# Optimization experiments

Hardware: AMD Instinct MI355X
Metric: run time of the kernel (lower is better)

## Reference

```python
import jax, jax.numpy as jnp
import numpy as np

B, NUM_OBJ, R, D, C = 1024, 128, 32, 512, 7  # scans, obj slots, rel samples, feat dim, rel classes
N = NUM_OBJ + R  # 160 graph nodes per scan


def setup_inputs() -> dict:
    key = jax.random.key(0)
    ks = jax.random.split(key, 8)
    obj_feats = jax.random.normal(ks[0], (B, NUM_OBJ, D), jnp.float32)
    pairs = jax.random.randint(ks[1], (B, R, 2), 0, NUM_OBJ, dtype=jnp.int32)
    init = lambda k, shape, fan_in: jax.random.normal(k, shape, jnp.float32) / np.float32(np.sqrt(fan_in))
    return {
        "obj_feats": obj_feats,
        "pairs": pairs,
        "fuse_w": init(ks[2], (2 * D, D), 2 * D), "fuse_b": jnp.zeros((D,), jnp.float32),
        "gcn_w": init(ks[3], (D, D), D), "gcn_b": jnp.zeros((D,), jnp.float32),
        "fc1_w": init(ks[4], (D, 256), D), "fc1_b": jnp.zeros((256,), jnp.float32),
        "fc2_w": init(ks[5], (256, 128), 256), "fc2_b": jnp.zeros((128,), jnp.float32),
        "fc3_w": init(ks[6], (128, C), 128), "fc3_b": jnp.zeros((C,), jnp.float32),
    }


def reference(obj_feats, pairs, fuse_w, fuse_b, gcn_w, gcn_b,
              fc1_w, fc1_b, fc2_w, fc2_b, fc3_w, fc3_b):
    # --- init_rel_node (pos_fuse=False): fuse sub/obj features per sampled pair ---
    sub = jnp.take_along_axis(obj_feats, pairs[:, :, 0:1], axis=1)  # [B,R,D]
    obj = jnp.take_along_axis(obj_feats, pairs[:, :, 1:2], axis=1)  # [B,R,D]
    init_rel = jnp.concatenate([sub, obj], axis=-1) @ fuse_w + fuse_b  # [B,R,D]

    # --- X: object node feats in rows [0,NUM_OBJ), rel node feats in rows [NUM_OBJ,N) ---
    X = jnp.concatenate([obj_feats, init_rel], axis=1)  # [B,N,D]

    # --- A: get_graph_gcn_with_rel -- scatter 4 directed edges per pair ---
    b_idx = jnp.arange(B)[:, None]                      # [B,1]
    ridx = NUM_OBJ + jnp.arange(R)[None, :]             # [1,R] rel node index j+num_obj
    p0, p1 = pairs[:, :, 0], pairs[:, :, 1]             # [B,R]
    A = jnp.zeros((B, N, N), jnp.float32)
    A = A.at[b_idx, p0, ridx].set(1.0)
    A = A.at[b_idx, ridx, p1].set(1.0)
    A = A.at[b_idx, p1, ridx].set(1.0)
    A = A.at[b_idx, ridx, p0].set(1.0)

    # --- simpleGCN: relu((A @ X) W + b) ---
    H = jax.nn.relu(jnp.einsum('bnm,bmd->bnd', A, X) @ gcn_w + gcn_b)  # [B,N,D]

    # --- residual: GCN rel-node output + init rel feats ---
    rel_feat = H[:, NUM_OBJ:, :] + init_rel  # [B,R,D]

    # --- proxi_detector (dropout = identity, eval behavior) ---
    h = jax.nn.relu(rel_feat @ fc1_w + fc1_b)
    h = jax.nn.relu(h @ fc2_w + fc2_b)
    logits = h @ fc3_w + fc3_b  # [B,R,C]
    return jax.nn.softmax(logits, axis=-1)
```

## Files before the change

### kernel.cpp

```cpp
#include <hip/hip_runtime.h>
#include <hip/hip_bf16.h>

#define B_    1024
#define NOBJ  128
#define RREL  32
#define DIM   512
#define MTOT  32768

typedef __bf16 bf16x8 __attribute__((ext_vector_type(8)));
typedef float  f32x4  __attribute__((ext_vector_type(4)));

__device__ __forceinline__ unsigned short f2bf(float f) {
    unsigned int u = __float_as_uint(f);
    u += 0x7FFFu + ((u >> 16) & 1u);
    return (unsigned short)(u >> 16);
}
__device__ __forceinline__ float bf2f(unsigned short h) {
    return __uint_as_float(((unsigned int)h) << 16);
}

__device__ __forceinline__ void load16_to_lds(const unsigned short* g, unsigned short* l) {
    __builtin_amdgcn_global_load_lds((const __attribute__((address_space(1))) void*)g,
                                     (__attribute__((address_space(3))) void*)l,
                                     16, 0, 0);
}

__global__ __launch_bounds__(256) void gather_kernel(
        const float* __restrict__ obj, const int* __restrict__ pairs,
        unsigned short* __restrict__ As, unsigned short* __restrict__ Msum) {
    int t = threadIdx.x;
    int base = blockIdx.x * 8;
    for (int rr = 0; rr < 8; ++rr) {
        int m  = base + rr;
        int b  = m >> 5;
        int p0 = pairs[(m << 1) + 0];
        int p1 = pairs[(m << 1) + 1];
        const float* srow = obj + (size_t)(b * NOBJ + p0) * DIM;
        const float* orow = obj + (size_t)(b * NOBJ + p1) * DIM;
        float2 s2 = *(const float2*)(srow + 2 * t);
        float2 o2 = *(const float2*)(orow + 2 * t);
        size_t arow = (size_t)m * 1024;
        *(ushort2*)(As + arow + 2 * t)       = make_ushort2(f2bf(s2.x), f2bf(s2.y));
        *(ushort2*)(As + arow + DIM + 2 * t) = make_ushort2(f2bf(o2.x), f2bf(o2.y));
        float mx = s2.x, my = s2.y;
        if (p0 != p1) { mx += o2.x; my += o2.y; }
        *(ushort2*)(Msum + (size_t)m * DIM + 2 * t) = make_ushort2(f2bf(mx), f2bf(my));
    }
}

__global__ __launch_bounds__(256) void transpose_w(
        const float* __restrict__ in, unsigned short* __restrict__ out,
        int K, int Nlog2) {
    int id = blockIdx.x * 256 + threadIdx.x;
    if (id >= (K << Nlog2)) return;
    int k = id >> Nlog2;
    int n = id & ((1 << Nlog2) - 1);
    out[(size_t)n * K + k] = f2bf(in[id]);
}

template<bool RELU, bool ADD, bool OUT_BF16>
__global__ __launch_bounds__(256) void gemm_bt(
        const unsigned short* __restrict__ A, const unsigned short* __restrict__ BT,
        const float* __restrict__ bias, const float* __restrict__ addsrc,
        void* __restrict__ outp, int KTOT, int NTOT) {
    __shared__ __align__(16) unsigned short ldsA[128 * 32];
    __shared__ __align__(16) unsigned short ldsB[128 * 32];

    int tid  = threadIdx.x;
    int wid  = tid >> 6;
    int lane = tid & 63;
    int wm   = wid & 1;
    int wn   = wid >> 1;
    int m0   = blockIdx.x * 128;
    int n0   = blockIdx.y * 128;

    f32x4 acc[4][4];
    for (int i = 0; i < 4; ++i)
        for (int j = 0; j < 4; ++j)
            for (int k = 0; k < 4; ++k) acc[i][j][k] = 0.0f;

    int r = tid >> 2, c = tid & 3;
    const unsigned short* ag0 = A  + (size_t)(m0 + r)      * KTOT + c * 8;
    const unsigned short* ag1 = A  + (size_t)(m0 + 64 + r) * KTOT + c * 8;
    const unsigned short* bg0 = BT + (size_t)(n0 + r)      * KTOT + c * 8;
    const unsigned short* bg1 = BT + (size_t)(n0 + 64 + r) * KTOT + c * 8;
    unsigned short* la0 = ldsA + wid * 512;
    unsigned short* la1 = ldsA + 2048 + wid * 512;
    unsigned short* lb0 = ldsB + wid * 512;
    unsigned short* lb1 = ldsB + 2048 + wid * 512;

    int arow = wm * 64 + (lane & 15);
    int brow = wn * 64 + (lane & 15);
    int koff = (lane >> 4) * 8;

    for (int k0 = 0; k0 < KTOT; k0 += 32) {
        __syncthreads();
        load16_to_lds(ag0 + k0, la0);
        load16_to_lds(ag1 + k0, la1);
        load16_to_lds(bg0 + k0, lb0);
        load16_to_lds(bg1 + k0, lb1);
        __syncthreads();

        bf16x8 a[4], b[4];
#pragma unroll
        for (int i = 0; i < 4; ++i)
            a[i] = *(const bf16x8*)(ldsA + (arow + i * 16) * 32 + koff);
#pragma unroll
        for (int j = 0; j < 4; ++j)
            b[j] = *(const bf16x8*)(ldsB + (brow + j * 16) * 32 + koff);
#pragma unroll
        for (int i = 0; i < 4; ++i)
#pragma unroll
            for (int j = 0; j < 4; ++j)
                acc[i][j] = __builtin_amdgcn_mfma_f32_16x16x32_bf16(a[i], b[j], acc[i][j], 0, 0, 0);
    }

    int crow  = wm * 64 + (lane >> 4) * 4;
    int ccol0 = wn * 64 + (lane & 15);
    float bcol[4];
#pragma unroll
    for (int j = 0; j < 4; ++j) bcol[j] = bias[n0 + ccol0 + j * 16];

#pragma unroll
    for (int i = 0; i < 4; ++i) {
#pragma unroll
        for (int j = 0; j < 4; ++j) {
            int col = n0 + ccol0 + j * 16;
#pragma unroll
            for (int jj = 0; jj < 4; ++jj) {
                int row = m0 + crow + i * 16 + jj;
                float v = acc[i][j][jj] + bcol[j];
                if (RELU) v = fmaxf(v, 0.0f);
                if (ADD)  v += addsrc[(size_t)row * NTOT + col];
                if (OUT_BF16)
                    ((unsigned short*)outp)[(size_t)row * NTOT + col] = f2bf(v);
                else
                    ((float*)outp)[(size_t)row * NTOT + col] = v;
            }
        }
    }
}

__global__ __launch_bounds__(256) void head_kernel(
        const unsigned short* __restrict__ h2, const float* __restrict__ w3,
        const float* __restrict__ b3, float* __restrict__ out) {
    __shared__ float w[128 * 7];
    __shared__ float bb[7];
    int t = threadIdx.x;
    for (int i = t; i < 128 * 7; i += 256) w[i] = w3[i];
    if (t < 7) bb[t] = b3[t];
    __syncthreads();

    int m = blockIdx.x * 256 + t;
    const uint2* hv = (const uint2*)(h2 + (size_t)m * 128);
    float accv[7];
#pragma unroll
    for (int cc = 0; cc < 7; ++cc) accv[cc] = bb[cc];
    for (int kk = 0; kk < 32; ++kk) {
        uint2 u = hv[kk];
        float f0 = bf2f((unsigned short)(u.x & 0xffff));
        float f1 = bf2f((unsigned short)(u.x >> 16));
        float f2 = bf2f((unsigned short)(u.y & 0xffff));
        float f3 = bf2f((unsigned short)(u.y >> 16));
        int k = kk * 4;
#pragma unroll
        for (int cc = 0; cc < 7; ++cc) {
            accv[cc] = fmaf(f0, w[(k + 0) * 7 + cc], accv[cc]);
            accv[cc] = fmaf(f1, w[(k + 1) * 7 + cc], accv[cc]);
            accv[cc] = fmaf(f2, w[(k + 2) * 7 + cc], accv[cc]);
            accv[cc] = fmaf(f3, w[(k + 3) * 7 + cc], accv[cc]);
        }
    }
    float mx = accv[0];
#pragma unroll
    for (int cc = 1; cc < 7; ++cc) mx = fmaxf(mx, accv[cc]);
    float sum = 0.f;
#pragma unroll
    for (int cc = 0; cc < 7; ++cc) { accv[cc] = expf(accv[cc] - mx); sum += accv[cc]; }
    float inv = 1.0f / sum;
#pragma unroll
    for (int cc = 0; cc < 7; ++cc) out[(size_t)m * 7 + cc] = accv[cc] * inv;
}

extern "C" void kernel_launch(void* const* d_in, const int* in_sizes, int n_in,
                              void* d_out, int out_size, void* d_ws, size_t ws_size,
                              hipStream_t stream) {
    (void)in_sizes; (void)n_in; (void)out_size; (void)ws_size;
    const float* obj    = (const float*)d_in[0];
    const int*   pairs  = (const int*)  d_in[1];
    const float* fuse_w = (const float*)d_in[2];
    const float* fuse_b = (const float*)d_in[3];
    const float* gcn_w  = (const float*)d_in[4];
    const float* gcn_b  = (const float*)d_in[5];
    const float* fc1_w  = (const float*)d_in[6];
    const float* fc1_b  = (const float*)d_in[7];
    const float* fc2_w  = (const float*)d_in[8];
    const float* fc2_b  = (const float*)d_in[9];
    const float* fc3_w  = (const float*)d_in[10];
    const float* fc3_b  = (const float*)d_in[11];
    float* out = (float*)d_out;

    char* ws = (char*)d_ws;
    unsigned short* As      = (unsigned short*)(ws);
    unsigned short* h1      = (unsigned short*)(ws);
    unsigned short* h2      = (unsigned short*)(ws + (16u << 20));
    unsigned short* rf      = (unsigned short*)(ws + (24u << 20));
    unsigned short* Msum    = (unsigned short*)(ws + (64u << 20));
    float*          initrel = (float*)         (ws + (96u << 20));
    unsigned short* WfT     = (unsigned short*)(ws + (160u << 20));
    unsigned short* WgT     = (unsigned short*)(ws + (161u << 20));
    unsigned short* W1T     = (unsigned short*)(ws + (162u << 20));
    unsigned short* W2T     = (unsigned short*)(ws + (163u << 20));

    gather_kernel<<<MTOT / 8, 256, 0, stream>>>(obj, pairs, As, Msum);
    transpose_w<<<(1024 * 512) / 256, 256, 0, stream>>>(fuse_w, WfT, 1024, 9);
    transpose_w<<<(512  * 512) / 256, 256, 0, stream>>>(gcn_w,  WgT, 512,  9);
    transpose_w<<<(512  * 256) / 256, 256, 0, stream>>>(fc1_w,  W1T, 512,  8);
    transpose_w<<<(256  * 128) / 256, 256, 0, stream>>>(fc2_w,  W2T, 256,  7);

    gemm_bt<false, false, false><<<dim3(MTOT / 128, 4), 256, 0, stream>>>(
        As, WfT, fuse_b, nullptr, initrel, 1024, 512);
    gemm_bt<true, true, true><<<dim3(MTOT / 128, 4), 256, 0, stream>>>(
        Msum, WgT, gcn_b, initrel, rf, 512, 512);
    gemm_bt<true, false, true><<<dim3(MTOT / 128, 2), 256, 0, stream>>>(
        rf, W1T, fc1_b, nullptr, h1, 512, 256);
    gemm_bt<true, false, true><<<dim3(MTOT / 128, 1), 256, 0, stream>>>(
        h1, W2T, fc2_b, nullptr, h2, 256, 128);
    head_kernel<<<MTOT / 256, 256, 0, stream>>>(h2, fc3_w, fc3_b, out);
}
```

Measured before the change: 501.0 us.

## Fuse fuse/GCN GEMMs and MLP head into two kernels, tile weight transposes

Merges the fuse-linear and GCN GEMMs into one kernel that keeps both accumulators in registers, so the fp32 init_rel intermediate is never written or re-read. Fuses fc1, fc2, fc3 and the softmax into a single tail kernel that keeps h1 and h2 in LDS, so those intermediates never go through global memory. Weight transposes now use a shared-memory 32x32 tile so both reads and writes are coalesced. The costs are doubled accumulator registers in the fused GEMM, which may cut occupancy, and a large LDS footprint in the tail kernel with fc1 tiles recomputed per 128-row block.

```diff
diff --git a/kernel.cpp b/kernel.cpp
--- a/kernel.cpp
+++ b/kernel.cpp
@@ -48,21 +48,29 @@
     }
 }
 
-__global__ __launch_bounds__(256) void transpose_w(
+__global__ __launch_bounds__(256) void transpose_tile(
         const float* __restrict__ in, unsigned short* __restrict__ out,
-        int K, int Nlog2) {
-    int id = blockIdx.x * 256 + threadIdx.x;
-    if (id >= (K << Nlog2)) return;
-    int k = id >> Nlog2;
-    int n = id & ((1 << Nlog2) - 1);
-    out[(size_t)n * K + k] = f2bf(in[id]);
-}
-
-template<bool RELU, bool ADD, bool OUT_BF16>
-__global__ __launch_bounds__(256) void gemm_bt(
-        const unsigned short* __restrict__ A, const unsigned short* __restrict__ BT,
-        const float* __restrict__ bias, const float* __restrict__ addsrc,
-        void* __restrict__ outp, int KTOT, int NTOT) {
+        int K, int N) {
+    __shared__ float t32[32][33];
+    int t  = threadIdx.x;
+    int tx = t & 31, ty = t >> 5;
+    int bk = blockIdx.x * 32, bn = blockIdx.y * 32;
+#pragma unroll
+    for (int i = 0; i < 4; ++i)
+        t32[ty + i * 8][tx] = in[(size_t)(bk + ty + i * 8) * N + bn + tx];
+    __syncthreads();
+#pragma unroll
+    for (int i = 0; i < 4; ++i)
+        out[(size_t)(bn + ty + i * 8) * K + bk + tx] = f2bf(t32[tx][ty + i * 8]);
+}
+
+__global__ __launch_bounds__(256) void gemm_fused12(
+        const unsigned short* __restrict__ As,
+        const unsigned short* __restrict__ Msum,
+        const unsigned short* __restrict__ WfT,
+        const unsigned short* __restrict__ WgT,
+        const float* __restrict__ fuse_b, const float* __restrict__ gcn_b,
+        unsigned short* __restrict__ rf) {
     __shared__ __align__(16) unsigned short ldsA[128 * 32];
     __shared__ __align__(16) unsigned short ldsB[128 * 32];
 
@@ -74,16 +82,15 @@
     int m0   = blockIdx.x * 128;
     int n0   = blockIdx.y * 128;
 
-    f32x4 acc[4][4];
-    for (int i = 0; i < 4; ++i)
+    f32x4 accF[4][4], accG[4][4];
+#pragma unroll
+    for (int i = 0; i < 4; ++i)
+#pragma unroll
         for (int j = 0; j < 4; ++j)
-            for (int k = 0; k < 4; ++k) acc[i][j][k] = 0.0f;
+#pragma unroll
+            for (int k = 0; k < 4; ++k) { accF[i][j][k] = 0.0f; accG[i][j][k] = 0.0f; }
 
     int r = tid >> 2, c = tid & 3;
-    const unsigned short* ag0 = A  + (size_t)(m0 + r)      * KTOT + c * 8;
-    const unsigned short* ag1 = A  + (size_t)(m0 + 64 + r) * KTOT + c * 8;
-    const unsigned short* bg0 = BT + (size_t)(n0 + r)      * KTOT + c * 8;
-    const unsigned short* bg1 = BT + (size_t)(n0 + 64 + r) * KTOT + c * 8;
     unsigned short* la0 = ldsA + wid * 512;
     unsigned short* la1 = ldsA + 2048 + wid * 512;
     unsigned short* lb0 = ldsB + wid * 512;
@@ -93,93 +100,235 @@
     int brow = wn * 64 + (lane & 15);
     int koff = (lane >> 4) * 8;
 
-    for (int k0 = 0; k0 < KTOT; k0 += 32) {
-        __syncthreads();
-        load16_to_lds(ag0 + k0, la0);
-        load16_to_lds(ag1 + k0, la1);
-        load16_to_lds(bg0 + k0, lb0);
-        load16_to_lds(bg1 + k0, lb1);
-        __syncthreads();
-
-        bf16x8 a[4], b[4];
-#pragma unroll
-        for (int i = 0; i < 4; ++i)
-            a[i] = *(const bf16x8*)(ldsA + (arow + i * 16) * 32 + koff);
-#pragma unroll
-        for (int j = 0; j < 4; ++j)
-            b[j] = *(const bf16x8*)(ldsB + (brow + j * 16) * 32 + koff);
-#pragma unroll
-        for (int i = 0; i < 4; ++i)
-#pragma unroll
-            for (int j = 0; j < 4; ++j)
-                acc[i][j] = __builtin_amdgcn_mfma_f32_16x16x32_bf16(a[i], b[j], acc[i][j], 0, 0, 0);
+    {
+        const unsigned short* ag0 = As + (size_t)(m0 + r)      * 1024 + c * 8;
+        const unsigned short* ag1 = As + (size_t)(m0 + 64 + r) * 1024 + c * 8;
+        const unsigned short* bg0 = WfT + (size_t)(n0 + r)      * 1024 + c * 8;
+        const unsigned short* bg1 = WfT + (size_t)(n0 + 64 + r) * 1024 + c * 8;
+        for (int k0 = 0; k0 < 1024; k0 += 32) {
+            __syncthreads();
+            load16_to_lds(ag0 + k0, la0);
+            load16_to_lds(ag1 + k0, la1);
+            load16_to_lds(bg0 + k0, lb0);
+            load16_to_lds(bg1 + k0, lb1);
+            __syncthreads();
+            bf16x8 a[4], b[4];
+#pragma unroll
+            for (int i = 0; i < 4; ++i)
+                a[i] = *(const bf16x8*)(ldsA + (arow + i * 16) * 32 + koff);
+#pragma unroll
+            for (int j = 0; j < 4; ++j)
+                b[j] = *(const bf16x8*)(ldsB + (brow + j * 16) * 32 + koff);
+#pragma unroll
+            for (int i = 0; i < 4; ++i)
+#pragma unroll
+                for (int j = 0; j < 4; ++j)
+                    accF[i][j] = __builtin_amdgcn_mfma_f32_16x16x32_bf16(a[i], b[j], accF[i][j], 0, 0, 0);
+        }
+    }
+    {
+        const unsigned short* ag0 = Msum + (size_t)(m0 + r)      * 512 + c * 8;
+        const unsigned short* ag1 = Msum + (size_t)(m0 + 64 + r) * 512 + c * 8;
+        const unsigned short* bg0 = WgT + (size_t)(n0 + r)      * 512 + c * 8;
+        const unsigned short* bg1 = WgT + (size_t)(n0 + 64 + r) * 512 + c * 8;
+        for (int k0 = 0; k0 < 512; k0 += 32) {
+            __syncthreads();
+            load16_to_lds(ag0 + k0, la0);
+            load16_to_lds(ag1 + k0, la1);
+            load16_to_lds(bg0 + k0, lb0);
+            load16_to_lds(bg1 + k0, lb1);
+            __syncthreads();
+            bf16x8 a[4], b[4];
+#pragma unroll
+            for (int i = 0; i < 4; ++i)
+                a[i] = *(const bf16x8*)(ldsA + (arow + i * 16) * 32 + koff);
+#pragma unroll
+            for (int j = 0; j < 4; ++j)
+                b[j] = *(const bf16x8*)(ldsB + (brow + j * 16) * 32 + koff);
+#pragma unroll
+            for (int i = 0; i < 4; ++i)
+#pragma unroll
+                for (int j = 0; j < 4; ++j)
+                    accG[i][j] = __builtin_amdgcn_mfma_f32_16x16x32_bf16(a[i], b[j], accG[i][j], 0, 0, 0);
+        }
     }
 
     int crow  = wm * 64 + (lane >> 4) * 4;
     int ccol0 = wn * 64 + (lane & 15);
-    float bcol[4];
-#pragma unroll
-    for (int j = 0; j < 4; ++j) bcol[j] = bias[n0 + ccol0 + j * 16];
-
-#pragma unroll
-    for (int i = 0; i < 4; ++i) {
+    float bf_[4], bg_[4];
+#pragma unroll
+    for (int j = 0; j < 4; ++j) {
+        bf_[j] = fuse_b[n0 + ccol0 + j * 16];
+        bg_[j] = gcn_b [n0 + ccol0 + j * 16];
+    }
+#pragma unroll
+    for (int i = 0; i < 4; ++i)
 #pragma unroll
         for (int j = 0; j < 4; ++j) {
             int col = n0 + ccol0 + j * 16;
 #pragma unroll
             for (int jj = 0; jj < 4; ++jj) {
                 int row = m0 + crow + i * 16 + jj;
-                float v = acc[i][j][jj] + bcol[j];
-                if (RELU) v = fmaxf(v, 0.0f);
-                if (ADD)  v += addsrc[(size_t)row * NTOT + col];
-                if (OUT_BF16)
-                    ((unsigned short*)outp)[(size_t)row * NTOT + col] = f2bf(v);
-                else
-                    ((float*)outp)[(size_t)row * NTOT + col] = v;
+                float v = fmaxf(accG[i][j][jj] + bg_[j], 0.0f) + accF[i][j][jj] + bf_[j];
+                rf[(size_t)row * 512 + col] = f2bf(v);
             }
         }
-    }
-}
-
-__global__ __launch_bounds__(256) void head_kernel(
-        const unsigned short* __restrict__ h2, const float* __restrict__ w3,
-        const float* __restrict__ b3, float* __restrict__ out) {
-    __shared__ float w[128 * 7];
-    __shared__ float bb[7];
-    int t = threadIdx.x;
-    for (int i = t; i < 128 * 7; i += 256) w[i] = w3[i];
-    if (t < 7) bb[t] = b3[t];
+}
+
+#define H1S 136
+__global__ __launch_bounds__(256) void tail_kernel(
+        const unsigned short* __restrict__ rf,
+        const unsigned short* __restrict__ W1T,
+        const unsigned short* __restrict__ W2T,
+        const float* __restrict__ b1, const float* __restrict__ b2,
+        const float* __restrict__ w3, const float* __restrict__ b3,
+        float* __restrict__ out) {
+    __shared__ __align__(16) unsigned short ldsA[128 * 32];
+    __shared__ __align__(16) unsigned short ldsB[128 * 32];
+    __shared__ __align__(16) unsigned short ldsH1[128 * H1S];
+    __shared__ __align__(16) unsigned short ldsH2[128 * H1S];
+    __shared__ float ldsW3[128 * 7];
+    __shared__ float ldsB3[7];
+
+    int tid  = threadIdx.x;
+    int wid  = tid >> 6;
+    int lane = tid & 63;
+    int wm   = wid & 1;
+    int wn   = wid >> 1;
+    int m0   = blockIdx.x * 128;
+
+    for (int i = tid; i < 128 * 7; i += 256) ldsW3[i] = w3[i];
+    if (tid < 7) ldsB3[tid] = b3[tid];
+
+    int r = tid >> 2, c = tid & 3;
+    unsigned short* la0 = ldsA + wid * 512;
+    unsigned short* la1 = ldsA + 2048 + wid * 512;
+    unsigned short* lb0 = ldsB + wid * 512;
+    unsigned short* lb1 = ldsB + 2048 + wid * 512;
+
+    int arow = wm * 64 + (lane & 15);
+    int brow = wn * 64 + (lane & 15);
+    int koff = (lane >> 4) * 8;
+    int crow  = wm * 64 + (lane >> 4) * 4;
+    int ccol0 = wn * 64 + (lane & 15);
+
+    const unsigned short* ag0 = rf + (size_t)(m0 + r)      * 512 + c * 8;
+    const unsigned short* ag1 = rf + (size_t)(m0 + 64 + r) * 512 + c * 8;
+
+    f32x4 acc2[4][4];
+#pragma unroll
+    for (int i = 0; i < 4; ++i)
+#pragma unroll
+        for (int j = 0; j < 4; ++j)
+#pragma unroll
+            for (int k = 0; k < 4; ++k) acc2[i][j][k] = 0.0f;
+
+    for (int nt = 0; nt < 2; ++nt) {
+        int n0 = nt * 128;
+        f32x4 acc1[4][4];
+#pragma unroll
+        for (int i = 0; i < 4; ++i)
+#pragma unroll
+            for (int j = 0; j < 4; ++j)
+#pragma unroll
+                for (int k = 0; k < 4; ++k) acc1[i][j][k] = 0.0f;
+
+        const unsigned short* bg0 = W1T + (size_t)(n0 + r)      * 512 + c * 8;
+        const unsigned short* bg1 = W1T + (size_t)(n0 + 64 + r) * 512 + c * 8;
+        for (int k0 = 0; k0 < 512; k0 += 32) {
+            __syncthreads();
+            load16_to_lds(ag0 + k0, la0);
+            load16_to_lds(ag1 + k0, la1);
+            load16_to_lds(bg0 + k0, lb0);
+            load16_to_lds(bg1 + k0, lb1);
+            __syncthreads();
+            bf16x8 a[4], b[4];
+#pragma unroll
+            for (int i = 0; i < 4; ++i)
+                a[i] = *(const bf16x8*)(ldsA + (arow + i * 16) * 32 + koff);
+#pragma unroll
+            for (int j = 0; j < 4; ++j)
+                b[j] = *(const bf16x8*)(ldsB + (brow + j * 16) * 32 + koff);
+#pragma unroll
+            for (int i = 0; i < 4; ++i)
+#pragma unroll
+                for (int j = 0; j < 4; ++j)
+                    acc1[i][j] = __builtin_amdgcn_mfma_f32_16x16x32_bf16(a[i], b[j], acc1[i][j], 0, 0, 0);
+        }
+        __syncthreads();
+#pragma unroll
+        for (int i = 0; i < 4; ++i)
+#pragma unroll
+            for (int j = 0; j < 4; ++j) {
+                int col = ccol0 + j * 16;
+                float bb = b1[n0 + col];
+#pragma unroll
+                for (int jj = 0; jj < 4; ++jj) {
+                    int row = crow + i * 16 + jj;
+                    float v = fmaxf(acc1[i][j][jj] + bb, 0.0f);
+                    ldsH1[row * H1S + col] = f2bf(v);
+                }
+            }
+        __syncthreads();
+        const unsigned short* wg0 = W2T + (size_t)r        * 256 + n0 + c * 8;
+        const unsigned short* wg1 = W2T + (size_t)(64 + r) * 256 + n0 + c * 8;
+        for (int k0 = 0; k0 < 128; k0 += 32) {
+            __syncthreads();
+            load16_to_lds(wg0 + k0, lb0);
+            load16_to_lds(wg1 + k0, lb1);
+            __syncthreads();
+            bf16x8 a[4], b[4];
+#pragma unroll
+            for (int i = 0; i < 4; ++i)
+                a[i] = *(const bf16x8*)(ldsH1 + (arow + i * 16) * H1S + k0 + koff);
+#pragma unroll
+            for (int j = 0; j < 4; ++j)
+                b[j] = *(const bf16x8*)(ldsB + (brow + j * 16) * 32 + koff);
+#pragma unroll
+            for (int i = 0; i < 4; ++i)
+#pragma unroll
+                for (int j = 0; j < 4; ++j)
+                    acc2[i][j] = __builtin_amdgcn_mfma_f32_16x16x32_bf16(a[i], b[j], acc2[i][j], 0, 0, 0);
+        }
+        __syncthreads();
+    }
+
+#pragma unroll
+    for (int i = 0; i < 4; ++i)
+#pragma unroll
+        for (int j = 0; j < 4; ++j) {
+            int col = ccol0 + j * 16;
+            float bb = b2[col];
+#pragma unroll
+            for (int jj = 0; jj < 4; ++jj) {
+                int row = crow + i * 16 + jj;
+                float v = fmaxf(acc2[i][j][jj] + bb, 0.0f);
+                ldsH2[row * H1S + col] = f2bf(v);
+            }
+        }
     __syncthreads();
 
-    int m = blockIdx.x * 256 + t;
-    const uint2* hv = (const uint2*)(h2 + (size_t)m * 128);
-    float accv[7];
-#pragma unroll
-    for (int cc = 0; cc < 7; ++cc) accv[cc] = bb[cc];
-    for (int kk = 0; kk < 32; ++kk) {
-        uint2 u = hv[kk];
-        float f0 = bf2f((unsigned short)(u.x & 0xffff));
-        float f1 = bf2f((unsigned short)(u.x >> 16));
-        float f2 = bf2f((unsigned short)(u.y & 0xffff));
-        float f3 = bf2f((unsigned short)(u.y >> 16));
-        int k = kk * 4;
-#pragma unroll
-        for (int cc = 0; cc < 7; ++cc) {
-            accv[cc] = fmaf(f0, w[(k + 0) * 7 + cc], accv[cc]);
-            accv[cc] = fmaf(f1, w[(k + 1) * 7 + cc], accv[cc]);
-            accv[cc] = fmaf(f2, w[(k + 2) * 7 + cc], accv[cc]);
-            accv[cc] = fmaf(f3, w[(k + 3) * 7 + cc], accv[cc]);
-        }
-    }
-    float mx = accv[0];
-#pragma unroll
-    for (int cc = 1; cc < 7; ++cc) mx = fmaxf(mx, accv[cc]);
-    float sum = 0.f;
-#pragma unroll
-    for (int cc = 0; cc < 7; ++cc) { accv[cc] = expf(accv[cc] - mx); sum += accv[cc]; }
-    float inv = 1.0f / sum;
-#pragma unroll
-    for (int cc = 0; cc < 7; ++cc) out[(size_t)m * 7 + cc] = accv[cc] * inv;
+    if (tid < 128) {
+        const unsigned short* hrow = ldsH2 + tid * H1S;
+        float accv[7];
+#pragma unroll
+        for (int cc = 0; cc < 7; ++cc) accv[cc] = ldsB3[cc];
+        for (int k = 0; k < 128; ++k) {
+            float f = bf2f(hrow[k]);
+#pragma unroll
+            for (int cc = 0; cc < 7; ++cc)
+                accv[cc] = fmaf(f, ldsW3[k * 7 + cc], accv[cc]);
+        }
+        float mx = accv[0];
+#pragma unroll
+        for (int cc = 1; cc < 7; ++cc) mx = fmaxf(mx, accv[cc]);
+        float sum = 0.f;
+#pragma unroll
+        for (int cc = 0; cc < 7; ++cc) { accv[cc] = __expf(accv[cc] - mx); sum += accv[cc]; }
+        float inv = 1.0f / sum;
+#pragma unroll
+        for (int cc = 0; cc < 7; ++cc) out[(size_t)(m0 + tid) * 7 + cc] = accv[cc] * inv;
+    }
 }
 
 extern "C" void kernel_launch(void* const* d_in, const int* in_sizes, int n_in,
@@ -201,30 +350,23 @@
     float* out = (float*)d_out;
 
     char* ws = (char*)d_ws;
-    unsigned short* As      = (unsigned short*)(ws);
-    unsigned short* h1      = (unsigned short*)(ws);
-    unsigned short* h2      = (unsigned short*)(ws + (16u << 20));
-    unsigned short* rf      = (unsigned short*)(ws + (24u << 20));
-    unsigned short* Msum    = (unsigned short*)(ws + (64u << 20));
-    float*          initrel = (float*)         (ws + (96u << 20));
-    unsigned short* WfT     = (unsigned short*)(ws + (160u << 20));
-    unsigned short* WgT     = (unsigned short*)(ws + (161u << 20));
-    unsigned short* W1T     = (unsigned short*)(ws + (162u << 20));
-    unsigned short* W2T     = (unsigned short*)(ws + (163u << 20));
+    unsigned short* As   = (unsigned short*)(ws);
+    unsigned short* Msum = (unsigned short*)(ws + (64u  << 20));
+    unsigned short* rf   = (unsigned short*)(ws + (96u  << 20));
+    unsigned short* WfT  = (unsigned short*)(ws + (128u << 20));
+    unsigned short* WgT  = (unsigned short*)(ws + (129u << 20));
+    unsigned short* W1T  = (unsigned short*)(ws + (130u << 20));
+    unsigned short* W2T  = (unsigned short*)(ws + (131u << 20));
 
     gather_kernel<<<MTOT / 8, 256, 0, stream>>>(obj, pairs, As, Msum);
-    transpose_w<<<(1024 * 512) / 256, 256, 0, stream>>>(fuse_w, WfT, 1024, 9);
-    transpose_w<<<(512  * 512) / 256, 256, 0, stream>>>(gcn_w,  WgT, 512,  9);
-    transpose_w<<<(512  * 256) / 256, 256, 0, stream>>>(fc1_w,  W1T, 512,  8);
-    transpose_w<<<(256  * 128) / 256, 256, 0, stream>>>(fc2_w,  W2T, 256,  7);
-
-    gemm_bt<false, false, false><<<dim3(MTOT / 128, 4), 256, 0, stream>>>(
-        As, WfT, fuse_b, nullptr, initrel, 1024, 512);
-    gemm_bt<true, true, true><<<dim3(MTOT / 128, 4), 256, 0, stream>>>(
-        Msum, WgT, gcn_b, initrel, rf, 512, 512);
-    gemm_bt<true, false, true><<<dim3(MTOT / 128, 2), 256, 0, stream>>>(
-        rf, W1T, fc1_b, nullptr, h1, 512, 256);
-    gemm_bt<true, false, true><<<dim3(MTOT / 128, 1), 256, 0, stream>>>(
-        h1, W2T, fc2_b, nullptr, h2, 256, 128);
-    head_kernel<<<MTOT / 256, 256, 0, stream>>>(h2, fc3_w, fc3_b, out);
-}
+    transpose_tile<<<dim3(1024 / 32, 512 / 32), 256, 0, stream>>>(fuse_w, WfT, 1024, 512);
+    transpose_tile<<<dim3(512  / 32, 512 / 32), 256, 0, stream>>>(gcn_w,  WgT, 512,  512);
+    transpose_tile<<<dim3(512  / 32, 256 / 32), 256, 0, stream>>>(fc1_w,  W1T, 512,  256);
+    transpose_tile<<<dim3(256  / 32, 128 / 32), 256, 0, stream>>>(fc2_w,  W2T, 256,  128);
+
+    gemm_fused12<<<dim3(MTOT / 128, 4), 256, 0, stream>>>(
+        As, Msum, WfT, WgT, fuse_b, gcn_b, rf);
+
+    tail_kernel<<<MTOT / 128, 256, 0, stream>>>(
+        rf, W1T, W2T, fc1_b, fc2_b, fc3_w, fc3_b, out);
+}
```

Measured after the change: 470.2 us. 6.2% less time.
